# Kernel tuning notes

Hardware: AMD Instinct MI355X
Metric: run time of the kernel (lower is better)

## Reference

```python
import jax, jax.numpy as jnp
import numpy as np

N, E, IN, H, OUT = 100000, 1600000, 128, 128, 64


def setup_inputs() -> dict:
    key = jax.random.key(0)
    ks = jax.random.split(key, 6)
    glorot = lambda k, i, o: jax.random.normal(k, (i, o), jnp.float32) * np.float32(np.sqrt(2.0 / (i + o)))
    return dict(
        x=jax.random.normal(ks[0], (N, IN), jnp.float32),
        edge_index=jax.random.randint(ks[1], (2, E), 0, N, dtype=jnp.int64 if jax.config.jax_enable_x64 else jnp.int32),
        W1=glorot(ks[2], IN, H), b1=jnp.zeros((H,), jnp.float32),
        W2=glorot(ks[3], H, H), b2=jnp.zeros((H,), jnp.float32),
        W3=glorot(ks[4], H, OUT), b3=jnp.zeros((OUT,), jnp.float32),
    )


def _gcn_norm(edge_index, num_nodes):
    # add self loops with weight 1.0 (GCNConv add_self_loops=True, edge_weight=None -> ones)
    loop = jnp.arange(num_nodes, dtype=edge_index.dtype)
    src = jnp.concatenate([edge_index[0], loop])
    dst = jnp.concatenate([edge_index[1], loop])
    ew = jnp.ones(src.shape, jnp.float32)
    deg = jax.ops.segment_sum(ew, dst, num_segments=num_nodes)  # in-degree on dst
    dinv = jnp.where(deg > 0, jax.lax.rsqrt(deg), 0.0)
    norm = dinv[src] * ew * dinv[dst]  # [E+N]
    return src, dst, norm


def _conv(x, src, dst, norm, W, b):
    h = x @ W                                        # linear transform first (GCNConv order)
    msg = h[src] * norm[:, None]                     # gather + scale, [E+N, F]
    agg = jax.ops.segment_sum(msg, dst, num_segments=x.shape[0])  # scatter-add
    return agg + b


def reference(x, edge_index, W1, b1, W2, b2, W3, b3):
    # eval-mode forward: dropout is identity
    src, dst, norm = _gcn_norm(edge_index, x.shape[0])  # same graph -> norm shared across layers
    h = jax.nn.relu(_conv(x, src, dst, norm, W1, b1))
    h = jax.nn.relu(_conv(h, src, dst, norm, W2, b2))
    h = _conv(h, src, dst, norm, W3, b3)
    return jax.nn.log_softmax(h, axis=-1)
```

## Files before the change

### kernel.cpp

```cpp
#include <hip/hip_runtime.h>

typedef unsigned int u32;
typedef unsigned short u16;
typedef unsigned char u8;
typedef __attribute__((ext_vector_type(8))) short short8;
typedef __attribute__((ext_vector_type(4))) float f32x4;
typedef __attribute__((ext_vector_type(2))) float f32x2;

#define MAXBIN 1024
#define SORT_TPB 1024

__device__ inline float bfu2f(u32 u) { return __builtin_bit_cast(float, u); }
__device__ inline u16 f2bf(float f) {
    u32 u = __builtin_bit_cast(u32, f);
    u32 r = (u + 0x7fffu + ((u >> 16) & 1u)) >> 16;
    return (u16)r;
}

__global__ __launch_bounds__(SORT_TPB) void k_bhist(const int* __restrict__ ei, int E, int W,
                                                    int* __restrict__ binTot, int NBIN) {
    __shared__ int h[MAXBIN];
    int tid = threadIdx.x;
    for (int i = tid; i < NBIN; i += SORT_TPB) h[i] = 0;
    __syncthreads();
    int s = blockIdx.x * W, e = min(E, s + W);
    for (int j = s + tid; j < e; j += SORT_TPB) atomicAdd(&h[ei[E + j] >> 7], 1);
    __syncthreads();
    for (int i = tid; i < NBIN; i += SORT_TPB) {
        int v = h[i];
        if (v) atomicAdd(&binTot[i], v);
    }
}

__global__ void k_bscan(const int* __restrict__ binTot, int NBIN,
                        int* __restrict__ binStart, int* __restrict__ binCur) {
    __shared__ int wsum[4];
    int t = threadIdx.x;
    int base = t * 4;
    int v0 = (base + 0 < NBIN) ? binTot[base + 0] : 0;
    int v1 = (base + 1 < NBIN) ? binTot[base + 1] : 0;
    int v2 = (base + 2 < NBIN) ? binTot[base + 2] : 0;
    int v3 = (base + 3 < NBIN) ? binTot[base + 3] : 0;
    int s = v0 + v1 + v2 + v3;
    int lane = t & 63, wv = t >> 6;
    int isc = s;
    for (int d = 1; d < 64; d <<= 1) { int o = __shfl_up(isc, d, 64); if (lane >= d) isc += o; }
    if (lane == 63) wsum[wv] = isc;
    __syncthreads();
    int woff = 0;
    for (int w = 0; w < wv; w++) woff += wsum[w];
    int run = woff + isc - s;
    if (base + 0 < NBIN) { binStart[base + 0] = run; binCur[base + 0] = run; } run += v0;
    if (base + 1 < NBIN) { binStart[base + 1] = run; binCur[base + 1] = run; } run += v1;
    if (base + 2 < NBIN) { binStart[base + 2] = run; binCur[base + 2] = run; } run += v2;
    if (base + 3 < NBIN) { binStart[base + 3] = run; binCur[base + 3] = run; }
    if (t == 255) binStart[NBIN] = wsum[0] + wsum[1] + wsum[2] + wsum[3];
}

__global__ __launch_bounds__(SORT_TPB) void k_bscatter(const int* __restrict__ ei, int E, int W,
                                                       int* __restrict__ binCur,
                                                       u32* __restrict__ binned, int NBIN) {
    __shared__ int lh[MAXBIN];
    __shared__ int lb[MAXBIN];
    int tid = threadIdx.x;
    for (int i = tid; i < NBIN; i += SORT_TPB) lh[i] = 0;
    __syncthreads();
    int s = blockIdx.x * W, e = min(E, s + W);
    for (int j = s + tid; j < e; j += SORT_TPB) atomicAdd(&lh[ei[E + j] >> 7], 1);
    __syncthreads();
    for (int i = tid; i < NBIN; i += SORT_TPB) {
        int h = lh[i];
        lb[i] = h ? atomicAdd(&binCur[i], h) : 0;
    }
    __syncthreads();
    for (int i = tid; i < NBIN; i += SORT_TPB) lh[i] = 0;
    __syncthreads();
    for (int j = s + tid; j < e; j += SORT_TPB) {
        int d = ei[E + j];
        int b = d >> 7;
        int r = atomicAdd(&lh[b], 1);
        binned[lb[b] + r] = ((u32)ei[j] << 7) | (u32)(d & 127);
    }
}

__global__ __launch_bounds__(256) void k_bcsr(const u32* __restrict__ binned,
                                              const int* __restrict__ binStart,
                                              int N, int E, int* __restrict__ offs,
                                              float* __restrict__ dinv,
                                              int* __restrict__ csr, int NBIN) {
    __shared__ int cnt[128];
    __shared__ int off[128];
    __shared__ int tot;
    int b = blockIdx.x;
    int tid = threadIdx.x;
    int dLo = b << 7;
    int nd = min(128, N - dLo);
    int e0 = binStart[b], e1 = binStart[b + 1];
    if (tid < 128) cnt[tid] = 0;
    __syncthreads();
    for (int j = e0 + tid; j < e1; j += 256) atomicAdd(&cnt[binned[j] & 127u], 1);
    __syncthreads();
    int c = (tid < 128) ? cnt[tid] : 0;
    int lane = tid & 63;
    int isc = c;
    for (int d = 1; d < 64; d <<= 1) { int o = __shfl_up(isc, d, 64); if (lane >= d) isc += o; }
    if (tid == 63) tot = isc;
    __syncthreads();
    int add = (tid >= 64 && tid < 128) ? tot : 0;
    if (tid < 128) off[tid] = add + isc - c;
    __syncthreads();
    if (tid < nd) {
        offs[dLo + tid] = e0 + off[tid];
        dinv[dLo + tid] = rsqrtf((float)(c + 1));
    }
    if (b == NBIN - 1 && tid == 0) offs[N] = E;
    if (tid < 128) cnt[tid] = 0;
    __syncthreads();
    for (int j = e0 + tid; j < e1; j += 256) {
        u32 v = binned[j];
        int d7 = (int)(v & 127u);
        int r = atomicAdd(&cnt[d7], 1);
        csr[e0 + off[d7] + r] = (int)(v >> 7);
    }
}

__global__ void k_wtall(const float* __restrict__ W1, const float* __restrict__ W2,
                        const float* __restrict__ W3, u16* __restrict__ wt1,
                        u16* __restrict__ wt2, u16* __restrict__ wt3) {
    int idx = blockIdx.x * 256 + threadIdx.x;
    if (idx < 16384) {
        int k = idx >> 7, m = idx & 127;
        wt1[m * 128 + k] = f2bf(W1[idx]);
    } else if (idx < 32768) {
        int i = idx - 16384, k = i >> 7, m = i & 127;
        wt2[m * 128 + k] = f2bf(W2[i]);
    } else if (idx < 40960) {
        int i = idx - 32768, k = i >> 6, m = i & 63;
        wt3[m * 128 + k] = f2bf(W3[i]);
    }
}

template <int M, bool F32IN>
__global__ __launch_bounds__(256) void k_gemm(const void* __restrict__ xin,
                                              const u16* __restrict__ wt,
                                              const float* __restrict__ dinv,
                                              u8* __restrict__ g8, int N) {
    constexpr int K = 128;
    constexpr int LDK = 136;
    __shared__ u16 lwt[M * LDK];
    int tid = threadIdx.x;
    const uint4* wsrc = (const uint4*)wt;
#pragma unroll
    for (int c = tid; c < M * K / 8; c += 256) {
        int row = c >> 4, kc = c & 15;
        *(uint4*)&lwt[row * LDK + kc * 8] = wsrc[c];
    }
    __syncthreads();
    int lane = tid & 63, wv = tid >> 6;
    int node = blockIdx.x * 64 + wv * 16 + (lane & 15);
    int nodec = min(node, N - 1);
    int kr = (lane >> 4) * 8;
    f32x4 acc[M / 16];
#pragma unroll
    for (int t = 0; t < M / 16; t++) acc[t] = (f32x4){0.f, 0.f, 0.f, 0.f};
#pragma unroll
    for (int ks = 0; ks < 4; ks++) {
        short8 bfr;
        if (F32IN) {
            const float* xr = (const float*)xin + (size_t)nodec * K + ks * 32 + kr;
            float4 fa = *(const float4*)xr;
            float4 fb = *(const float4*)(xr + 4);
            bfr = (short8){(short)f2bf(fa.x), (short)f2bf(fa.y), (short)f2bf(fa.z),
                           (short)f2bf(fa.w), (short)f2bf(fb.x), (short)f2bf(fb.y),
                           (short)f2bf(fb.z), (short)f2bf(fb.w)};
        } else {
            bfr = *(const short8*)((const u16*)xin + (size_t)nodec * K + ks * 32 + kr);
        }
#pragma unroll
        for (int t = 0; t < M / 16; t++) {
            short8 afr = *(const short8*)&lwt[(t * 16 + (lane & 15)) * LDK + ks * 32 + kr];
            acc[t] = __builtin_amdgcn_mfma_f32_16x16x32_bf16(afr, bfr, acc[t], 0, 0, 0);
        }
    }
    if (node < N) {
        float dv16 = dinv[node] * 16.0f;
        int r0 = (lane >> 4) * 4;
#pragma unroll
        for (int t = 0; t < M / 16; t++) {
            u32 w = __builtin_amdgcn_cvt_pk_fp8_f32(acc[t][0] * dv16, acc[t][1] * dv16, 0, false);
            w = __builtin_amdgcn_cvt_pk_fp8_f32(acc[t][2] * dv16, acc[t][3] * dv16, w, true);
            *(u32*)(g8 + (size_t)node * M + t * 16 + r0) = w;
        }
    }
}

__global__ __launch_bounds__(256) void k_agg128(const u8* __restrict__ g8,
                                                const int* __restrict__ offs,
                                                const int* __restrict__ csr,
                                                const float* __restrict__ dinv,
                                                const float* __restrict__ bias,
                                                u16* __restrict__ hout, int N) {
    int wid = (blockIdx.x * 256 + threadIdx.x) >> 6;
    if (wid >= N) return;
    int lane = threadIdx.x & 63;
    int q = lane >> 4;
    int f = lane & 15;
    int s = offs[wid], e = offs[wid + 1];
    const u8* gf = g8 + f * 8;
    f32x2 a01 = {0.f, 0.f}, a23 = {0.f, 0.f}, a45 = {0.f, 0.f}, a67 = {0.f, 0.f};
    int em1 = e - 1;
    for (int j = s; j < e; j += 16) {
        int b4 = j + q * 4;
        int i1 = b4 + 1, i2 = b4 + 2, i3 = b4 + 3;
        int s0 = csr[min(b4, em1)];
        int s1 = csr[min(i1, em1)];
        int s2 = csr[min(i2, em1)];
        int s3 = csr[min(i3, em1)];
        uint2 w0 = *(const uint2*)(gf + ((u32)s0 << 7));
        uint2 w1 = *(const uint2*)(gf + ((u32)s1 << 7));
        uint2 w2 = *(const uint2*)(gf + ((u32)s2 << 7));
        uint2 w3 = *(const uint2*)(gf + ((u32)s3 << 7));
        if (b4 >= e) { w0.x = 0u; w0.y = 0u; }
        if (i1 >= e) { w1.x = 0u; w1.y = 0u; }
        if (i2 >= e) { w2.x = 0u; w2.y = 0u; }
        if (i3 >= e) { w3.x = 0u; w3.y = 0u; }
        f32x2 t0, t1;
        t0 = __builtin_amdgcn_cvt_pk_f32_fp8((int)w0.x, false) +
             __builtin_amdgcn_cvt_pk_f32_fp8((int)w1.x, false);
        t1 = __builtin_amdgcn_cvt_pk_f32_fp8((int)w2.x, false) +
             __builtin_amdgcn_cvt_pk_f32_fp8((int)w3.x, false);
        a01 += t0 + t1;
        t0 = __builtin_amdgcn_cvt_pk_f32_fp8((int)w0.x, true) +
             __builtin_amdgcn_cvt_pk_f32_fp8((int)w1.x, true);
        t1 = __builtin_amdgcn_cvt_pk_f32_fp8((int)w2.x, true) +
             __builtin_amdgcn_cvt_pk_f32_fp8((int)w3.x, true);
        a23 += t0 + t1;
        t0 = __builtin_amdgcn_cvt_pk_f32_fp8((int)w0.y, false) +
             __builtin_amdgcn_cvt_pk_f32_fp8((int)w1.y, false);
        t1 = __builtin_amdgcn_cvt_pk_f32_fp8((int)w2.y, false) +
             __builtin_amdgcn_cvt_pk_f32_fp8((int)w3.y, false);
        a45 += t0 + t1;
        t0 = __builtin_amdgcn_cvt_pk_f32_fp8((int)w0.y, true) +
             __builtin_amdgcn_cvt_pk_f32_fp8((int)w1.y, true);
        t1 = __builtin_amdgcn_cvt_pk_f32_fp8((int)w2.y, true) +
             __builtin_amdgcn_cvt_pk_f32_fp8((int)w3.y, true);
        a67 += t0 + t1;
    }
    float a[8] = {a01.x, a01.y, a23.x, a23.y, a45.x, a45.y, a67.x, a67.y};
#pragma unroll
    for (int i = 0; i < 8; i++) {
        a[i] += __shfl_xor(a[i], 16, 64);
        a[i] += __shfl_xor(a[i], 32, 64);
    }
    if (lane < 16) {
        float sc = dinv[wid] * 0.0625f;
        uint2 sp = *(const uint2*)(g8 + (size_t)wid * 128 + f * 8);
        f32x2 s01 = __builtin_amdgcn_cvt_pk_f32_fp8((int)sp.x, false);
        f32x2 s23 = __builtin_amdgcn_cvt_pk_f32_fp8((int)sp.x, true);
        f32x2 s45 = __builtin_amdgcn_cvt_pk_f32_fp8((int)sp.y, false);
        f32x2 s67 = __builtin_amdgcn_cvt_pk_f32_fp8((int)sp.y, true);
        float sv[8] = {s01.x, s01.y, s23.x, s23.y, s45.x, s45.y, s67.x, s67.y};
        float4 b0 = *(const float4*)(bias + f * 8);
        float4 b1 = *(const float4*)(bias + f * 8 + 4);
        float bv[8] = {b0.x, b0.y, b0.z, b0.w, b1.x, b1.y, b1.z, b1.w};
        u32 o[4];
#pragma unroll
        for (int i = 0; i < 4; i++) {
            float v0 = fmaxf(fmaf(a[2 * i] + sv[2 * i], sc, bv[2 * i]), 0.f);
            float v1 = fmaxf(fmaf(a[2 * i + 1] + sv[2 * i + 1], sc, bv[2 * i + 1]), 0.f);
            o[i] = (u32)f2bf(v0) | ((u32)f2bf(v1) << 16);
        }
        *(uint4*)&hout[(size_t)wid * 128 + f * 8] = make_uint4(o[0], o[1], o[2], o[3]);
    }
}

__global__ __launch_bounds__(256) void k_agg64(const u8* __restrict__ g8,
                                               const int* __restrict__ offs,
                                               const int* __restrict__ csr,
                                               const float* __restrict__ dinv,
                                               const float* __restrict__ bias,
                                               float* __restrict__ out, int N) {
    int wid = (blockIdx.x * 256 + threadIdx.x) >> 6;
    if (wid >= N) return;
    int lane = threadIdx.x & 63;
    int q = lane >> 4;
    int f = lane & 15;
    int s = offs[wid], e = offs[wid + 1];
    const u8* gf = g8 + f * 4;
    f32x2 a01 = {0.f, 0.f}, a23 = {0.f, 0.f};
    int em1 = e - 1;
    for (int j = s; j < e; j += 16) {
        int b4 = j + q * 4;
        int i1 = b4 + 1, i2 = b4 + 2, i3 = b4 + 3;
        int s0 = csr[min(b4, em1)];
        int s1 = csr[min(i1, em1)];
        int s2 = csr[min(i2, em1)];
        int s3 = csr[min(i3, em1)];
        u32 w0 = *(const u32*)(gf + ((u32)s0 << 6));
        u32 w1 = *(const u32*)(gf + ((u32)s1 << 6));
        u32 w2 = *(const u32*)(gf + ((u32)s2 << 6));
        u32 w3 = *(const u32*)(gf + ((u32)s3 << 6));
        if (b4 >= e) w0 = 0u;
        if (i1 >= e) w1 = 0u;
        if (i2 >= e) w2 = 0u;
        if (i3 >= e) w3 = 0u;
        f32x2 t0 = __builtin_amdgcn_cvt_pk_f32_fp8((int)w0, false) +
                   __builtin_amdgcn_cvt_pk_f32_fp8((int)w1, false);
        f32x2 t1 = __builtin_amdgcn_cvt_pk_f32_fp8((int)w2, false) +
                   __builtin_amdgcn_cvt_pk_f32_fp8((int)w3, false);
        a01 += t0 + t1;
        t0 = __builtin_amdgcn_cvt_pk_f32_fp8((int)w0, true) +
             __builtin_amdgcn_cvt_pk_f32_fp8((int)w1, true);
        t1 = __builtin_amdgcn_cvt_pk_f32_fp8((int)w2, true) +
             __builtin_amdgcn_cvt_pk_f32_fp8((int)w3, true);
        a23 += t0 + t1;
    }
    float a[4] = {a01.x, a01.y, a23.x, a23.y};
#pragma unroll
    for (int i = 0; i < 4; i++) {
        a[i] += __shfl_xor(a[i], 16, 64);
        a[i] += __shfl_xor(a[i], 32, 64);
    }
    if (lane < 16) {
        float sc = dinv[wid] * 0.0625f;
        u32 sp = *(const u32*)(g8 + (size_t)wid * 64 + f * 4);
        f32x2 s01 = __builtin_amdgcn_cvt_pk_f32_fp8((int)sp, false);
        f32x2 s23 = __builtin_amdgcn_cvt_pk_f32_fp8((int)sp, true);
        float4 bb = *(const float4*)(bias + f * 4);
        float v0 = fmaf(a[0] + s01.x, sc, bb.x);
        float v1 = fmaf(a[1] + s01.y, sc, bb.y);
        float v2 = fmaf(a[2] + s23.x, sc, bb.z);
        float v3 = fmaf(a[3] + s23.y, sc, bb.w);
        float m = fmaxf(fmaxf(v0, v1), fmaxf(v2, v3));
#pragma unroll
        for (int d = 8; d >= 1; d >>= 1) m = fmaxf(m, __shfl_xor(m, d, 64));
        float ssum = __expf(v0 - m) + __expf(v1 - m) + __expf(v2 - m) + __expf(v3 - m);
#pragma unroll
        for (int d = 8; d >= 1; d >>= 1) ssum += __shfl_xor(ssum, d, 64);
        float lg = m + __logf(ssum);
        *(float4*)&out[(size_t)wid * 64 + f * 4] =
            make_float4(v0 - lg, v1 - lg, v2 - lg, v3 - lg);
    }
}

extern "C" void kernel_launch(void* const* d_in, const int* in_sizes, int n_in,
                              void* d_out, int out_size, void* d_ws, size_t ws_size,
                              hipStream_t stream) {
    const float* x  = (const float*)d_in[0];
    const int*   ei = (const int*)d_in[1];
    const float* W1 = (const float*)d_in[2];
    const float* b1 = (const float*)d_in[3];
    const float* W2 = (const float*)d_in[4];
    const float* b2 = (const float*)d_in[5];
    const float* W3 = (const float*)d_in[6];
    const float* b3 = (const float*)d_in[7];
    const int N = in_sizes[0] / 128;
    const int E = in_sizes[1] / 2;
    const int NBIN = (N + 127) >> 7;

    char* ws = (char*)d_ws;
    size_t o = 0;
    auto alloc = [&](size_t bytes) -> char* {
        char* p = ws + o;
        o += (bytes + 255) & ~(size_t)255;
        return p;
    };
    int*   binTot = (int*)alloc((size_t)MAXBIN * 4);
    int*   binSt  = (int*)alloc((size_t)(MAXBIN + 1) * 4);
    int*   binCur = (int*)alloc((size_t)MAXBIN * 4);
    float* dinv   = (float*)alloc((size_t)N * 4);
    int*   offs   = (int*)alloc((size_t)(N + 1) * 4);
    int*   csr    = (int*)alloc((size_t)E * 4);
    u16*   wt1    = (u16*)alloc(128 * 128 * 2);
    u16*   wt2    = (u16*)alloc(128 * 128 * 2);
    u16*   wt3    = (u16*)alloc(64 * 128 * 2);
    u8*    g8     = (u8*)alloc((size_t)N * 128);
    u16*   hbuf   = (u16*)alloc((size_t)N * 128 * 2);
    u32*   binned = (u32*)hbuf;
    float* outp   = (float*)d_out;

    hipMemsetAsync(binTot, 0, (size_t)MAXBIN * 4, stream);
    int W256 = (E + 255) / 256;
    k_bhist<<<256, SORT_TPB, 0, stream>>>(ei, E, W256, binTot, NBIN);
    k_bscan<<<1, 256, 0, stream>>>(binTot, NBIN, binSt, binCur);
    k_bscatter<<<256, SORT_TPB, 0, stream>>>(ei, E, W256, binCur, binned, NBIN);
    k_bcsr<<<NBIN, 256, 0, stream>>>(binned, binSt, N, E, offs, dinv, csr, NBIN);
    k_wtall<<<(40960 + 255) / 256, 256, 0, stream>>>(W1, W2, W3, wt1, wt2, wt3);

    int gG = (N + 63) / 64;
    int gA = (int)(((size_t)N * 64 + 255) / 256);

    k_gemm<128, true ><<<gG, 256, 0, stream>>>(x,    wt1, dinv, g8, N);
    k_agg128<<<gA, 256, 0, stream>>>(g8, offs, csr, dinv, b1, hbuf, N);
    k_gemm<128, false><<<gG, 256, 0, stream>>>(hbuf, wt2, dinv, g8, N);
    k_agg128<<<gA, 256, 0, stream>>>(g8, offs, csr, dinv, b2, hbuf, N);
    k_gemm<64,  false><<<gG, 256, 0, stream>>>(hbuf, wt3, dinv, g8, N);
    k_agg64<<<gA, 256, 0, stream>>>(g8, offs, csr, dinv, b3, outp, N);
}
```

Baseline: 317.7 us.

## Reduce FP8 neighbor gathers with MFMA selector matrix instead of scalar converts

```diff
diff --git a/kernel.cpp b/kernel.cpp
--- a/kernel.cpp
+++ b/kernel.cpp
@@ -3,6 +3,7 @@
 typedef unsigned int u32;
 typedef unsigned short u16;
 typedef unsigned char u8;
+typedef long i64;
 typedef __attribute__((ext_vector_type(8))) short short8;
 typedef __attribute__((ext_vector_type(4))) float f32x4;
 typedef __attribute__((ext_vector_type(2))) float f32x2;
@@ -10,11 +11,19 @@
 #define MAXBIN 1024
 #define SORT_TPB 1024
 
-__device__ inline float bfu2f(u32 u) { return __builtin_bit_cast(float, u); }
 __device__ inline u16 f2bf(float f) {
     u32 u = __builtin_bit_cast(u32, f);
     u32 r = (u + 0x7fffu + ((u >> 16) & 1u)) >> 16;
     return (u16)r;
+}
+
+__device__ inline f32x4 mfma_fp8(uint2 a, uint2 b, f32x4 c) {
+    return __builtin_amdgcn_mfma_f32_16x16x32_fp8_fp8(
+        __builtin_bit_cast(i64, a), __builtin_bit_cast(i64, b), c, 0, 0, 0);
+}
+
+__device__ inline int permP(int p) {
+    return ((p >> 5) << 5) + ((p & 3) << 3) + ((p >> 2) & 7);
 }
 
 __global__ __launch_bounds__(SORT_TPB) void k_bhist(const int* __restrict__ ei, int E, int W,
@@ -132,11 +141,11 @@
         int k = idx >> 7, m = idx & 127;
         wt1[m * 128 + k] = f2bf(W1[idx]);
     } else if (idx < 32768) {
-        int i = idx - 16384, k = i >> 7, m = i & 127;
-        wt2[m * 128 + k] = f2bf(W2[i]);
+        int i = idx - 16384, p = i >> 7, m = i & 127;
+        wt2[m * 128 + p] = f2bf(W2[permP(p) * 128 + m]);
     } else if (idx < 40960) {
-        int i = idx - 32768, k = i >> 6, m = i & 63;
-        wt3[m * 128 + k] = f2bf(W3[i]);
+        int i = idx - 32768, p = i >> 6, m = i & 63;
+        wt3[m * 128 + p] = f2bf(W3[permP(p) * 64 + m]);
     }
 }
 
@@ -206,13 +215,20 @@
     int q = lane >> 4;
     int f = lane & 15;
     int s = offs[wid], e = offs[wid + 1];
+    uint2 bsel;
+    bsel.x = (f < 4) ? (0x38u << (8 * f)) : 0u;
+    bsel.y = (f >= 4 && f < 8) ? (0x38u << (8 * (f - 4))) : 0u;
     const u8* gf = g8 + f * 8;
-    f32x2 a01 = {0.f, 0.f}, a23 = {0.f, 0.f}, a45 = {0.f, 0.f}, a67 = {0.f, 0.f};
+    f32x4 ac0 = {0.f, 0.f, 0.f, 0.f}, ac1 = ac0, ac2 = ac0, ac3 = ac0;
+    {
+        uint2 w = make_uint2(0u, 0u);
+        if (q == 0) w = *(const uint2*)(gf + ((u32)wid << 7));
+        ac0 = mfma_fp8(w, bsel, ac0);
+    }
     int em1 = e - 1;
     for (int j = s; j < e; j += 16) {
-        int b4 = j + q * 4;
-        int i1 = b4 + 1, i2 = b4 + 2, i3 = b4 + 3;
-        int s0 = csr[min(b4, em1)];
+        int i0 = j + q, i1 = j + 4 + q, i2 = j + 8 + q, i3 = j + 12 + q;
+        int s0 = csr[min(i0, em1)];
         int s1 = csr[min(i1, em1)];
         int s2 = csr[min(i2, em1)];
         int s3 = csr[min(i3, em1)];
@@ -220,57 +236,31 @@
         uint2 w1 = *(const uint2*)(gf + ((u32)s1 << 7));
         uint2 w2 = *(const uint2*)(gf + ((u32)s2 << 7));
         uint2 w3 = *(const uint2*)(gf + ((u32)s3 << 7));
-        if (b4 >= e) { w0.x = 0u; w0.y = 0u; }
+        if (i0 >= e) { w0.x = 0u; w0.y = 0u; }
         if (i1 >= e) { w1.x = 0u; w1.y = 0u; }
         if (i2 >= e) { w2.x = 0u; w2.y = 0u; }
         if (i3 >= e) { w3.x = 0u; w3.y = 0u; }
-        f32x2 t0, t1;
-        t0 = __builtin_amdgcn_cvt_pk_f32_fp8((int)w0.x, false) +
-             __builtin_amdgcn_cvt_pk_f32_fp8((int)w1.x, false);
-        t1 = __builtin_amdgcn_cvt_pk_f32_fp8((int)w2.x, false) +
-             __builtin_amdgcn_cvt_pk_f32_fp8((int)w3.x, false);
-        a01 += t0 + t1;
-        t0 = __builtin_amdgcn_cvt_pk_f32_fp8((int)w0.x, true) +
-             __builtin_amdgcn_cvt_pk_f32_fp8((int)w1.x, true);
-        t1 = __builtin_amdgcn_cvt_pk_f32_fp8((int)w2.x, true) +
-             __builtin_amdgcn_cvt_pk_f32_fp8((int)w3.x, true);
-        a23 += t0 + t1;
-        t0 = __builtin_amdgcn_cvt_pk_f32_fp8((int)w0.y, false) +
-             __builtin_amdgcn_cvt_pk_f32_fp8((int)w1.y, false);
-        t1 = __builtin_amdgcn_cvt_pk_f32_fp8((int)w2.y, false) +
-             __builtin_amdgcn_cvt_pk_f32_fp8((int)w3.y, false);
-        a45 += t0 + t1;
-        t0 = __builtin_amdgcn_cvt_pk_f32_fp8((int)w0.y, true) +
-             __builtin_amdgcn_cvt_pk_f32_fp8((int)w1.y, true);
-        t1 = __builtin_amdgcn_cvt_pk_f32_fp8((int)w2.y, true) +
-             __builtin_amdgcn_cvt_pk_f32_fp8((int)w3.y, true);
-        a67 += t0 + t1;
-    }
-    float a[8] = {a01.x, a01.y, a23.x, a23.y, a45.x, a45.y, a67.x, a67.y};
-#pragma unroll
-    for (int i = 0; i < 8; i++) {
-        a[i] += __shfl_xor(a[i], 16, 64);
-        a[i] += __shfl_xor(a[i], 32, 64);
-    }
-    if (lane < 16) {
+        ac0 = mfma_fp8(w0, bsel, ac0);
+        ac1 = mfma_fp8(w1, bsel, ac1);
+        ac2 = mfma_fp8(w2, bsel, ac2);
+        ac3 = mfma_fp8(w3, bsel, ac3);
+    }
+    f32x4 a = (ac0 + ac1) + (ac2 + ac3);
+    int jn = lane & 15, fq = lane >> 4;
+    if (jn < 8) {
         float sc = dinv[wid] * 0.0625f;
-        uint2 sp = *(const uint2*)(g8 + (size_t)wid * 128 + f * 8);
-        f32x2 s01 = __builtin_amdgcn_cvt_pk_f32_fp8((int)sp.x, false);
-        f32x2 s23 = __builtin_amdgcn_cvt_pk_f32_fp8((int)sp.x, true);
-        f32x2 s45 = __builtin_amdgcn_cvt_pk_f32_fp8((int)sp.y, false);
-        f32x2 s67 = __builtin_amdgcn_cvt_pk_f32_fp8((int)sp.y, true);
-        float sv[8] = {s01.x, s01.y, s23.x, s23.y, s45.x, s45.y, s67.x, s67.y};
-        float4 b0 = *(const float4*)(bias + f * 8);
-        float4 b1 = *(const float4*)(bias + f * 8 + 4);
-        float bv[8] = {b0.x, b0.y, b0.z, b0.w, b1.x, b1.y, b1.z, b1.w};
-        u32 o[4];
-#pragma unroll
-        for (int i = 0; i < 4; i++) {
-            float v0 = fmaxf(fmaf(a[2 * i] + sv[2 * i], sc, bv[2 * i]), 0.f);
-            float v1 = fmaxf(fmaf(a[2 * i + 1] + sv[2 * i + 1], sc, bv[2 * i + 1]), 0.f);
-            o[i] = (u32)f2bf(v0) | ((u32)f2bf(v1) << 16);
-        }
-        *(uint4*)&hout[(size_t)wid * 128 + f * 8] = make_uint4(o[0], o[1], o[2], o[3]);
+        u32 o0, o1;
+        {
+            float v0 = fmaxf(fmaf(a[0], sc, bias[(4 * fq + 0) * 8 + jn]), 0.f);
+            float v1 = fmaxf(fmaf(a[1], sc, bias[(4 * fq + 1) * 8 + jn]), 0.f);
+            o0 = (u32)f2bf(v0) | ((u32)f2bf(v1) << 16);
+        }
+        {
+            float v2 = fmaxf(fmaf(a[2], sc, bias[(4 * fq + 2) * 8 + jn]), 0.f);
+            float v3 = fmaxf(fmaf(a[3], sc, bias[(4 * fq + 3) * 8 + jn]), 0.f);
+            o1 = (u32)f2bf(v2) | ((u32)f2bf(v3) << 16);
+        }
+        *(uint2*)&hout[(size_t)wid * 128 + fq * 32 + jn * 4] = make_uint2(o0, o1);
     }
 }
 
@@ -280,66 +270,76 @@
                                                const float* __restrict__ dinv,
                                                const float* __restrict__ bias,
                                                float* __restrict__ out, int N) {
+    __shared__ float sm[4][64];
     int wid = (blockIdx.x * 256 + threadIdx.x) >> 6;
     if (wid >= N) return;
     int lane = threadIdx.x & 63;
+    int wv = (int)(threadIdx.x >> 6);
     int q = lane >> 4;
     int f = lane & 15;
+    bool frow = (f < 8);
     int s = offs[wid], e = offs[wid + 1];
-    const u8* gf = g8 + f * 4;
-    f32x2 a01 = {0.f, 0.f}, a23 = {0.f, 0.f};
+    uint2 bsel;
+    bsel.x = (f < 4) ? (0x38u << (8 * f)) : 0u;
+    bsel.y = (f >= 4 && f < 8) ? (0x38u << (8 * (f - 4))) : 0u;
+    const u8* gf = g8 + f * 8;
+    f32x4 ac0 = {0.f, 0.f, 0.f, 0.f}, ac1 = ac0, ac2 = ac0, ac3 = ac0;
+    {
+        uint2 w = make_uint2(0u, 0u);
+        if (q == 0 && frow) w = *(const uint2*)(gf + ((u32)wid << 6));
+        ac0 = mfma_fp8(w, bsel, ac0);
+    }
     int em1 = e - 1;
     for (int j = s; j < e; j += 16) {
-        int b4 = j + q * 4;
-        int i1 = b4 + 1, i2 = b4 + 2, i3 = b4 + 3;
-        int s0 = csr[min(b4, em1)];
+        int i0 = j + q, i1 = j + 4 + q, i2 = j + 8 + q, i3 = j + 12 + q;
+        int s0 = csr[min(i0, em1)];
         int s1 = csr[min(i1, em1)];
         int s2 = csr[min(i2, em1)];
         int s3 = csr[min(i3, em1)];
-        u32 w0 = *(const u32*)(gf + ((u32)s0 << 6));
-        u32 w1 = *(const u32*)(gf + ((u32)s1 << 6));
-        u32 w2 = *(const u32*)(gf + ((u32)s2 << 6));
-        u32 w3 = *(const u32*)(gf + ((u32)s3 << 6));
-        if (b4 >= e) w0 = 0u;
-        if (i1 >= e) w1 = 0u;
-        if (i2 >= e) w2 = 0u;
-        if (i3 >= e) w3 = 0u;
-        f32x2 t0 = __builtin_amdgcn_cvt_pk_f32_fp8((int)w0, false) +
-                   __builtin_amdgcn_cvt_pk_f32_fp8((int)w1, false);
-        f32x2 t1 = __builtin_amdgcn_cvt_pk_f32_fp8((int)w2, false) +
-                   __builtin_amdgcn_cvt_pk_f32_fp8((int)w3, false);
-        a01 += t0 + t1;
-        t0 = __builtin_amdgcn_cvt_pk_f32_fp8((int)w0, true) +
-             __builtin_amdgcn_cvt_pk_f32_fp8((int)w1, true);
-        t1 = __builtin_amdgcn_cvt_pk_f32_fp8((int)w2, true) +
-             __builtin_amdgcn_cvt_pk_f32_fp8((int)w3, true);
-        a23 += t0 + t1;
-    }
-    float a[4] = {a01.x, a01.y, a23.x, a23.y};
-#pragma unroll
-    for (int i = 0; i < 4; i++) {
-        a[i] += __shfl_xor(a[i], 16, 64);
-        a[i] += __shfl_xor(a[i], 32, 64);
+        uint2 w0 = make_uint2(0u, 0u), w1 = w0, w2 = w0, w3 = w0;
+        if (frow) {
+            w0 = *(const uint2*)(gf + ((u32)s0 << 6));
+            w1 = *(const uint2*)(gf + ((u32)s1 << 6));
+            w2 = *(const uint2*)(gf + ((u32)s2 << 6));
+            w3 = *(const uint2*)(gf + ((u32)s3 << 6));
+        }
+        if (i0 >= e) { w0.x = 0u; w0.y = 0u; }
+        if (i1 >= e) { w1.x = 0u; w1.y = 0u; }
+        if (i2 >= e) { w2.x = 0u; w2.y = 0u; }
+        if (i3 >= e) { w3.x = 0u; w3.y = 0u; }
+        ac0 = mfma_fp8(w0, bsel, ac0);
+        ac1 = mfma_fp8(w1, bsel, ac1);
+        ac2 = mfma_fp8(w2, bsel, ac2);
+        ac3 = mfma_fp8(w3, bsel, ac3);
+    }
+    f32x4 a = (ac0 + ac1) + (ac2 + ac3);
+    int jn = lane & 15, fq = lane >> 4;
+    bool act = (jn < 8) && (fq < 2);
+    if (act) {
+        float sc = dinv[wid] * 0.0625f;
+        float v0 = fmaf(a[0], sc, bias[(4 * fq + 0) * 8 + jn]);
+        float v1 = fmaf(a[1], sc, bias[(4 * fq + 1) * 8 + jn]);
+        float v2 = fmaf(a[2], sc, bias[(4 * fq + 2) * 8 + jn]);
+        float v3 = fmaf(a[3], sc, bias[(4 * fq + 3) * 8 + jn]);
+        float m = fmaxf(fmaxf(v0, v1), fmaxf(v2, v3));
+        m = fmaxf(m, __shfl_xor(m, 1, 64));
+        m = fmaxf(m, __shfl_xor(m, 2, 64));
+        m = fmaxf(m, __shfl_xor(m, 4, 64));
+        m = fmaxf(m, __shfl_xor(m, 16, 64));
+        float ss = __expf(v0 - m) + __expf(v1 - m) + __expf(v2 - m) + __expf(v3 - m);
+        ss += __shfl_xor(ss, 1, 64);
+        ss += __shfl_xor(ss, 2, 64);
+        ss += __shfl_xor(ss, 4, 64);
+        ss += __shfl_xor(ss, 16, 64);
+        float lg = m + __logf(ss);
+        sm[wv][(4 * fq + 0) * 8 + jn] = v0 - lg;
+        sm[wv][(4 * fq + 1) * 8 + jn] = v1 - lg;
+        sm[wv][(4 * fq + 2) * 8 + jn] = v2 - lg;
+        sm[wv][(4 * fq + 3) * 8 + jn] = v3 - lg;
     }
     if (lane < 16) {
-        float sc = dinv[wid] * 0.0625f;
-        u32 sp = *(const u32*)(g8 + (size_t)wid * 64 + f * 4);
-        f32x2 s01 = __builtin_amdgcn_cvt_pk_f32_fp8((int)sp, false);
-        f32x2 s23 = __builtin_amdgcn_cvt_pk_f32_fp8((int)sp, true);
-        float4 bb = *(const float4*)(bias + f * 4);
-        float v0 = fmaf(a[0] + s01.x, sc, bb.x);
-        float v1 = fmaf(a[1] + s01.y, sc, bb.y);
-        float v2 = fmaf(a[2] + s23.x, sc, bb.z);
-        float v3 = fmaf(a[3] + s23.y, sc, bb.w);
-        float m = fmaxf(fmaxf(v0, v1), fmaxf(v2, v3));
-#pragma unroll
-        for (int d = 8; d >= 1; d >>= 1) m = fmaxf(m, __shfl_xor(m, d, 64));
-        float ssum = __expf(v0 - m) + __expf(v1 - m) + __expf(v2 - m) + __expf(v3 - m);
-#pragma unroll
-        for (int d = 8; d >= 1; d >>= 1) ssum += __shfl_xor(ssum, d, 64);
-        float lg = m + __logf(ssum);
-        *(float4*)&out[(size_t)wid * 64 + f * 4] =
-            make_float4(v0 - lg, v1 - lg, v2 - lg, v3 - lg);
+        float4 ov = *(float4*)&sm[wv][lane * 4];
+        *(float4*)&out[(size_t)wid * 64 + lane * 4] = ov;
     }
 }
 
```

Result: faster. 308.7 us (-2.8%).
